# Performance work log

Measured on AMD Instinct MI355X. Metric: run time of the kernel, lower is better.

Reference implementation:

```python
import jax, jax.numpy as jnp
import numpy as np

U_DIM = 2048
V_DIM = 2048
LATENT = 2048
BATCH = 8192
SLOPE = 0.001  # LeakyReLU negative slope
EPS = 1e-5     # torch LayerNorm default eps


def layer_norm(x, gamma, beta):
    mu = jnp.mean(x, axis=-1, keepdims=True)
    var = jnp.var(x, axis=-1, keepdims=True)
    return (x - mu) * jax.lax.rsqrt(var + EPS) * gamma + beta


def leaky_relu(x):
    return jnp.where(x >= 0, x, SLOPE * x)


def setup_inputs() -> dict:
    key = jax.random.key(0)
    ks = jax.random.split(key, 6)
    u = jax.random.normal(ks[0], (BATCH, V_DIM), dtype=jnp.float32)
    v = jax.random.normal(ks[1], (BATCH, U_DIM), dtype=jnp.float32)
    # LayerNorm affine params (torch default: weight=1, bias=0 at init; randomize slightly)
    ln_u_w = jnp.ones((V_DIM,), jnp.float32)
    ln_u_b = jnp.zeros((V_DIM,), jnp.float32)
    ln_v_w = jnp.ones((U_DIM,), jnp.float32)
    ln_v_b = jnp.zeros((U_DIM,), jnp.float32)
    # Linear params (Kaiming-uniform-like scale)
    su = 1.0 / np.sqrt(V_DIM)
    sv = 1.0 / np.sqrt(U_DIM)
    W_u = jax.random.uniform(ks[2], (V_DIM, LATENT), jnp.float32, -su, su)
    b_u = jax.random.uniform(ks[3], (LATENT,), jnp.float32, -su, su)
    W_v = jax.random.uniform(ks[4], (U_DIM, LATENT), jnp.float32, -sv, sv)
    b_v = jax.random.uniform(ks[5], (LATENT,), jnp.float32, -sv, sv)
    return {"u": u, "v": v, "ln_u_w": ln_u_w, "ln_u_b": ln_u_b,
            "ln_v_w": ln_v_w, "ln_v_b": ln_v_b,
            "W_u": W_u, "b_u": b_u, "W_v": W_v, "b_v": b_v}


def reference(u, v, ln_u_w, ln_u_b, ln_v_w, ln_v_b, W_u, b_u, W_v, b_v):
    # u tower: LayerNorm -> Linear -> LeakyReLU
    hu = leaky_relu(layer_norm(u, ln_u_w, ln_u_b) @ W_u + b_u)   # [B, latent]
    # v tower: LayerNorm -> Linear -> LeakyReLU
    hv = leaky_relu(layer_norm(v, ln_v_w, ln_v_b) @ W_v + b_v)   # [B, latent]
    # dot-product reduction per row
    return jnp.sum(hu * hv, axis=-1)                              # [B]
```

## Files before the change

### kernel.cpp

```cpp
#include <hip/hip_runtime.h>

typedef unsigned short u16;
typedef __attribute__((ext_vector_type(8))) short short8;
typedef __attribute__((ext_vector_type(16))) float f32x16;

#define DIM 2048
#define NROWS 8192
#define SLOPE 0.001f
#define LN_EPS 1e-5f

#define LN_BLOCKS 4096
#define WT_BLOCKS 2048

#define BM 128
#define BN 256
#define BK 64
#define NT (DIM / BK)
#define TAUMAX (2 * NT)

__device__ __forceinline__ u16 f2bf(float f) {
    unsigned int u = __float_as_uint(f);
    u += 0x7FFFu + ((u >> 16) & 1u);
    return (u16)(u >> 16);
}

__device__ __forceinline__ void gload_lds16(const void* g, void* l) {
    __builtin_amdgcn_global_load_lds(
        (const __attribute__((address_space(1))) void*)g,
        (__attribute__((address_space(3))) void*)l, 16, 0, 0);
}

__global__ __launch_bounds__(256) void prep_kernel(
    const float* __restrict__ u, const float* __restrict__ v,
    const float* __restrict__ lnu_w, const float* __restrict__ lnu_b,
    const float* __restrict__ lnv_w, const float* __restrict__ lnv_b,
    const float* __restrict__ Wu, const float* __restrict__ Wv,
    u16* __restrict__ Au, u16* __restrict__ Av,
    u16* __restrict__ WtU, u16* __restrict__ WtV,
    float* __restrict__ out)
{
    __shared__ u16 tile[64][66];

    if (blockIdx.x < NROWS / 256)
        out[(blockIdx.x << 8) | threadIdx.x] = 0.f;

    if (blockIdx.x < LN_BLOCKS) {
        const int wave = threadIdx.x >> 6;
        const int lane = threadIdx.x & 63;
        const int r = blockIdx.x * 4 + wave;
        const bool isv = r >= NROWS;
        const int row = isv ? (r - NROWS) : r;
        const float* __restrict__ src = (isv ? v : u) + (size_t)row * DIM;
        const float* __restrict__ gw = isv ? lnv_w : lnu_w;
        const float* __restrict__ gb = isv ? lnv_b : lnu_b;
        u16* __restrict__ dst = (isv ? Av : Au) + (size_t)row * DIM;

        float4 x[8];
        #pragma unroll
        for (int i = 0; i < 8; ++i)
            x[i] = *(const float4*)(src + i * 256 + lane * 4);

        float s = 0.f, s2 = 0.f;
        #pragma unroll
        for (int i = 0; i < 8; ++i) {
            s  += (x[i].x + x[i].y) + (x[i].z + x[i].w);
            s2 += x[i].x*x[i].x + x[i].y*x[i].y + x[i].z*x[i].z + x[i].w*x[i].w;
        }
        #pragma unroll
        for (int m = 1; m < 64; m <<= 1) {
            s  += __shfl_xor(s, m);
            s2 += __shfl_xor(s2, m);
        }
        const float mu = s * (1.0f / DIM);
        const float rstd = rsqrtf(s2 * (1.0f / DIM) - mu * mu + LN_EPS);

        #pragma unroll
        for (int i = 0; i < 8; ++i) {
            const float4 w4 = *(const float4*)(gw + i * 256 + lane * 4);
            const float4 b4 = *(const float4*)(gb + i * 256 + lane * 4);
            union { u16 us[4]; uint2 v2; } pk;
            pk.us[0] = f2bf((x[i].x - mu) * rstd * w4.x + b4.x);
            pk.us[1] = f2bf((x[i].y - mu) * rstd * w4.y + b4.y);
            pk.us[2] = f2bf((x[i].z - mu) * rstd * w4.z + b4.z);
            pk.us[3] = f2bf((x[i].w - mu) * rstd * w4.w + b4.w);
            *(uint2*)(dst + i * 256 + lane * 4) = pk.v2;
        }
    } else {
        const int b = blockIdx.x - LN_BLOCKS;
        const int tower = b >> 10;
        const int t6 = b & 1023;
        const int n0 = (t6 & 31) * 64;
        const int k0 = (t6 >> 5) * 64;
        const float* __restrict__ src = tower ? Wv : Wu;
        u16* __restrict__ dst = tower ? WtV : WtU;
        const int c  = threadIdx.x & 15;
        const int rq = threadIdx.x >> 4;

        #pragma unroll
        for (int i = 0; i < 4; ++i) {
            const int k = rq + 16 * i;
            const float4 w = *(const float4*)(src + (size_t)(k0 + k) * DIM + n0 + c * 4);
            union { u16 us[4]; uint2 v2; } pk;
            pk.us[0] = f2bf(w.x); pk.us[1] = f2bf(w.y);
            pk.us[2] = f2bf(w.z); pk.us[3] = f2bf(w.w);
            *(uint2*)&tile[k][c * 4] = pk.v2;
        }
        __syncthreads();
        #pragma unroll
        for (int i = 0; i < 4; ++i) {
            const int n = rq + 16 * i;
            union { u16 us[4]; uint2 v2; } pk;
            #pragma unroll
            for (int j = 0; j < 4; ++j) pk.us[j] = tile[c * 4 + j][n];
            *(uint2*)(dst + (size_t)(n0 + n) * DIM + k0 + c * 4) = pk.v2;
        }
    }
}

__global__ __launch_bounds__(512) void fused_gemm_dot(
    const u16* __restrict__ Au, const u16* __restrict__ Av,
    const u16* __restrict__ WtU, const u16* __restrict__ WtV,
    const float* __restrict__ b_u, const float* __restrict__ b_v,
    float* __restrict__ out)
{
    __shared__ __align__(16) u16 smA[3][BM * BK];
    __shared__ __align__(16) u16 smB[3][BN * BK];

    const int tid   = threadIdx.x;
    const int wave  = tid >> 6;
    const int lane  = tid & 63;
    const int l31   = lane & 31;
    const int khalf = lane >> 5;
    const int wr    = wave >> 2;
    const int wc    = wave & 3;
    const int srow  = lane >> 3;
    const int gsw   = ((lane & 7) ^ srow ^ wave) * 8;

    const size_t arow0 = (size_t)blockIdx.x * BM;
    const size_t ncol0 = (size_t)blockIdx.y * BN;

#define STAGE_A(bi, tau) do {                                                      \
        const u16* As_ = (((tau) >> 5) ? Av : Au) + arow0 * DIM + ((tau)&31)*BK;   \
        _Pragma("unroll")                                                          \
        for (int i_ = 0; i_ < 2; ++i_) {                                           \
            const int rg_ = i_ * 64 + wave * 8;                                    \
            gload_lds16(As_ + (size_t)(rg_ + srow) * DIM + gsw,                    \
                        &smA[bi][rg_ * BK]);                                       \
        }                                                                          \
    } while (0)

#define STAGE_B(bi, tau, I0, I1) do {                                              \
        const u16* Bs_ = (((tau) >> 5) ? WtV : WtU) + ncol0 * DIM + ((tau)&31)*BK; \
        _Pragma("unroll")                                                          \
        for (int i_ = (I0); i_ < (I1); ++i_) {                                     \
            const int rg_ = i_ * 64 + wave * 8;                                    \
            gload_lds16(Bs_ + (size_t)(rg_ + srow) * DIM + gsw,                    \
                        &smB[bi][rg_ * BK]);                                       \
        }                                                                          \
    } while (0)

#define LDFRAGS(sa_, sb_, KK, X) do {                                              \
        const int cb_ = (KK) * 2 + khalf;                                          \
        _Pragma("unroll")                                                          \
        for (int mi_ = 0; mi_ < 2; ++mi_) {                                        \
            const int row_ = wr * 64 + mi_ * 32 + l31;                             \
            const int sl_ = cb_ ^ (row_ & 7) ^ ((row_ >> 3) & 7);                  \
            af[mi_][X] = *(const short8*)((sa_) + row_ * BK + sl_ * 8);            \
        }                                                                          \
        _Pragma("unroll")                                                          \
        for (int ni_ = 0; ni_ < 2; ++ni_) {                                        \
            const int row_ = wc * 64 + ni_ * 32 + l31;                             \
            const int sl_ = cb_ ^ (row_ & 7) ^ ((row_ >> 3) & 7);                  \
            bf[ni_][X] = *(const short8*)((sb_) + row_ * BK + sl_ * 8);            \
        }                                                                          \
    } while (0)

#define MFMA8() do {                                                               \
        __builtin_amdgcn_s_setprio(1);                                             \
        _Pragma("unroll")                                                          \
        for (int x_ = 0; x_ < 2; ++x_)                                             \
            _Pragma("unroll")                                                      \
            for (int mi_ = 0; mi_ < 2; ++mi_)                                      \
                _Pragma("unroll")                                                  \
                for (int ni_ = 0; ni_ < 2; ++ni_)                                  \
                    acc[mi_][ni_] = __builtin_amdgcn_mfma_f32_32x32x16_bf16(       \
                        af[mi_][x_], bf[ni_][x_], acc[mi_][ni_], 0, 0, 0);         \
        __builtin_amdgcn_s_setprio(0);                                             \
    } while (0)

    f32x16 acc[2][2];
    unsigned int hu_pk[2][2][8];

    STAGE_A(0, 0); STAGE_B(0, 0, 0, 4);
    STAGE_A(1, 1); STAGE_B(1, 1, 0, 4);

    int cur = 0;
    #pragma unroll
    for (int tower = 0; tower < 2; ++tower) {
        #pragma unroll
        for (int mi = 0; mi < 2; ++mi)
            #pragma unroll
            for (int ni = 0; ni < 2; ++ni)
                #pragma unroll
                for (int r = 0; r < 16; ++r)
                    acc[mi][ni][r] = 0.f;

        #pragma unroll 1
        for (int t = 0; t < NT; ++t) {
            const int tau = tower * NT + t;
            if (tau == TAUMAX - 1) asm volatile("s_waitcnt vmcnt(0)" ::: "memory");
            else                   asm volatile("s_waitcnt vmcnt(6)" ::: "memory");
            __builtin_amdgcn_s_barrier();
            asm volatile("" ::: "memory");

            const u16* sa = &smA[cur][0];
            const u16* sb = &smB[cur][0];
            int nb = cur + 2; if (nb >= 3) nb -= 3;
            short8 af[2][2], bf[2][2];

            LDFRAGS(sa, sb, 0, 0);
            LDFRAGS(sa, sb, 1, 1);
            if (tau + 2 < TAUMAX) { STAGE_A(nb, tau + 2); STAGE_B(nb, tau + 2, 0, 2); }
            __builtin_amdgcn_s_barrier();
            MFMA8();
            __builtin_amdgcn_s_barrier();
            LDFRAGS(sa, sb, 2, 0);
            LDFRAGS(sa, sb, 3, 1);
            if (tau + 2 < TAUMAX) STAGE_B(nb, tau + 2, 2, 4);
            __builtin_amdgcn_s_barrier();
            MFMA8();

            cur = (cur == 2) ? 0 : cur + 1;
        }

        if (tower == 0) {
            #pragma unroll
            for (int ni = 0; ni < 2; ++ni) {
                const float bias = b_u[ncol0 + wc * 64 + ni * 32 + l31];
                #pragma unroll
                for (int mi = 0; mi < 2; ++mi) {
                    #pragma unroll
                    for (int p = 0; p < 8; ++p) {
                        float h0 = acc[mi][ni][p * 2] + bias;
                        float h1 = acc[mi][ni][p * 2 + 1] + bias;
                        h0 = h0 >= 0.f ? h0 : SLOPE * h0;
                        h1 = h1 >= 0.f ? h1 : SLOPE * h1;
                        hu_pk[mi][ni][p] = (unsigned)f2bf(h0) | ((unsigned)f2bf(h1) << 16);
                    }
                }
            }
        }
    }

    #pragma unroll
    for (int mi = 0; mi < 2; ++mi) {
        #pragma unroll
        for (int rg = 0; rg < 4; ++rg) {
            float rsum[4] = {0.f, 0.f, 0.f, 0.f};
            #pragma unroll
            for (int ni = 0; ni < 2; ++ni) {
                const float bias = b_v[ncol0 + wc * 64 + ni * 32 + l31];
                #pragma unroll
                for (int r = 0; r < 4; ++r) {
                    const int reg = rg * 4 + r;
                    float hv = acc[mi][ni][reg] + bias;
                    hv = hv >= 0.f ? hv : SLOPE * hv;
                    const unsigned pk = hu_pk[mi][ni][reg >> 1];
                    const unsigned bits = (reg & 1) ? (pk & 0xFFFF0000u) : (pk << 16);
                    rsum[r] += __uint_as_float(bits) * hv;
                }
            }
            #pragma unroll
            for (int r = 0; r < 4; ++r) {
                const int reg = rg * 4 + r;
                float vsum = rsum[r];
                vsum += __shfl_xor(vsum, 1);
                vsum += __shfl_xor(vsum, 2);
                vsum += __shfl_xor(vsum, 4);
                vsum += __shfl_xor(vsum, 8);
                vsum += __shfl_xor(vsum, 16);
                if (l31 == 0) {
                    const int row = (int)arow0 + wr * 64 + mi * 32
                                  + (reg & 3) + 8 * (reg >> 2) + 4 * khalf;
                    atomicAdd(out + row, vsum);
                }
            }
        }
    }
#undef STAGE_A
#undef STAGE_B
#undef LDFRAGS
#undef MFMA8
}

extern "C" void kernel_launch(void* const* d_in, const int* in_sizes, int n_in,
                              void* d_out, int out_size, void* d_ws, size_t ws_size,
                              hipStream_t stream)
{
    const float* u     = (const float*)d_in[0];
    const float* v     = (const float*)d_in[1];
    const float* lnu_w = (const float*)d_in[2];
    const float* lnu_b = (const float*)d_in[3];
    const float* lnv_w = (const float*)d_in[4];
    const float* lnv_b = (const float*)d_in[5];
    const float* W_u   = (const float*)d_in[6];
    const float* b_u   = (const float*)d_in[7];
    const float* W_v   = (const float*)d_in[8];
    const float* b_v   = (const float*)d_in[9];
    float* out = (float*)d_out;

    char* ws = (char*)d_ws;
    u16* Au  = (u16*)(ws);
    u16* Av  = (u16*)(ws + (size_t)NROWS * DIM * 2);
    u16* WtU = (u16*)(ws + (size_t)NROWS * DIM * 4);
    u16* WtV = (u16*)(ws + (size_t)NROWS * DIM * 4 + (size_t)DIM * DIM * 2);

    prep_kernel<<<LN_BLOCKS + WT_BLOCKS, 256, 0, stream>>>(
        u, v, lnu_w, lnu_b, lnv_w, lnv_b, W_u, W_v, Au, Av, WtU, WtV, out);
    fused_gemm_dot<<<dim3(NROWS / BM, DIM / BN), 512, 0, stream>>>(
        Au, Av, WtU, WtV, b_u, b_v, out);
}
```

Baseline: 339.1 us.

## Enlarge GEMM tile to 256x256 with finer-grained phased staging pipeline

```diff
diff --git a/kernel.cpp b/kernel.cpp
--- a/kernel.cpp
+++ b/kernel.cpp
@@ -12,7 +12,7 @@
 #define LN_BLOCKS 4096
 #define WT_BLOCKS 2048
 
-#define BM 128
+#define BM 256
 #define BN 256
 #define BK 64
 #define NT (DIM / BK)
@@ -117,14 +117,14 @@
     }
 }
 
-__global__ __launch_bounds__(512) void fused_gemm_dot(
+__global__ __launch_bounds__(512, 2) void fused_gemm_dot(
     const u16* __restrict__ Au, const u16* __restrict__ Av,
     const u16* __restrict__ WtU, const u16* __restrict__ WtV,
     const float* __restrict__ b_u, const float* __restrict__ b_v,
     float* __restrict__ out)
 {
     __shared__ __align__(16) u16 smA[3][BM * BK];
-    __shared__ __align__(16) u16 smB[3][BN * BK];
+    __shared__ __align__(16) u16 smB[2][BN * BK];
 
     const int tid   = threadIdx.x;
     const int wave  = tid >> 6;
@@ -136,109 +136,120 @@
     const int srow  = lane >> 3;
     const int gsw   = ((lane & 7) ^ srow ^ wave) * 8;
 
-    const size_t arow0 = (size_t)blockIdx.x * BM;
-    const size_t ncol0 = (size_t)blockIdx.y * BN;
-
-#define STAGE_A(bi, tau) do {                                                      \
-        const u16* As_ = (((tau) >> 5) ? Av : Au) + arow0 * DIM + ((tau)&31)*BK;   \
-        _Pragma("unroll")                                                          \
-        for (int i_ = 0; i_ < 2; ++i_) {                                           \
-            const int rg_ = i_ * 64 + wave * 8;                                    \
-            gload_lds16(As_ + (size_t)(rg_ + srow) * DIM + gsw,                    \
-                        &smA[bi][rg_ * BK]);                                       \
+    const int bid = blockIdx.x;
+    const int bn  = bid & 7;
+    const int bm  = bid >> 3;
+    const size_t arow0 = (size_t)bm * BM;
+    const size_t ncol0 = (size_t)bn * BN;
+
+#define STAGE_A(T, buf, h) do {                                                    \
+        const u16* as_ = (((T) >= NT) ? Av : Au) + arow0 * DIM                     \
+                         + (size_t)((T) & (NT - 1)) * BK;                          \
+        _Pragma("unroll")                                                          \
+        for (int i2_ = 0; i2_ < 2; ++i2_) {                                        \
+            const int rg_ = (h) * 128 + i2_ * 64 + wave * 8;                       \
+            gload_lds16(as_ + (size_t)(rg_ + srow) * DIM + gsw,                    \
+                        &smA[buf][rg_ * BK]);                                      \
         }                                                                          \
     } while (0)
 
-#define STAGE_B(bi, tau, I0, I1) do {                                              \
-        const u16* Bs_ = (((tau) >> 5) ? WtV : WtU) + ncol0 * DIM + ((tau)&31)*BK; \
-        _Pragma("unroll")                                                          \
-        for (int i_ = (I0); i_ < (I1); ++i_) {                                     \
-            const int rg_ = i_ * 64 + wave * 8;                                    \
-            gload_lds16(Bs_ + (size_t)(rg_ + srow) * DIM + gsw,                    \
-                        &smB[bi][rg_ * BK]);                                       \
+#define STAGE_B(T, h) do {                                                         \
+        const u16* bs_ = (((T) >= NT) ? WtV : WtU) + ncol0 * DIM                   \
+                         + (size_t)((T) & (NT - 1)) * BK;                          \
+        _Pragma("unroll")                                                          \
+        for (int i2_ = 0; i2_ < 2; ++i2_) {                                        \
+            const int rg_ = (h) * 128 + i2_ * 64 + wave * 8;                       \
+            gload_lds16(bs_ + (size_t)(rg_ + srow) * DIM + gsw,                    \
+                        &smB[(T) & 1][rg_ * BK]);                                  \
         }                                                                          \
     } while (0)
 
-#define LDFRAGS(sa_, sb_, KK, X) do {                                              \
-        const int cb_ = (KK) * 2 + khalf;                                          \
-        _Pragma("unroll")                                                          \
-        for (int mi_ = 0; mi_ < 2; ++mi_) {                                        \
-            const int row_ = wr * 64 + mi_ * 32 + l31;                             \
+#define PHASE(AB, BB, KS, STAGE_STMT) do {                                         \
+        const u16* sa_ = &smA[AB][0];                                              \
+        const u16* sb_ = &smB[BB][0];                                              \
+        const int cb_ = (KS) * 2 + khalf;                                          \
+        short8 af_[4], bf_[2];                                                     \
+        _Pragma("unroll")                                                          \
+        for (int mi_ = 0; mi_ < 4; ++mi_) {                                        \
+            const int row_ = wr * 128 + mi_ * 32 + l31;                            \
             const int sl_ = cb_ ^ (row_ & 7) ^ ((row_ >> 3) & 7);                  \
-            af[mi_][X] = *(const short8*)((sa_) + row_ * BK + sl_ * 8);            \
+            af_[mi_] = *(const short8*)(sa_ + row_ * BK + sl_ * 8);                \
         }                                                                          \
         _Pragma("unroll")                                                          \
         for (int ni_ = 0; ni_ < 2; ++ni_) {                                        \
             const int row_ = wc * 64 + ni_ * 32 + l31;                             \
             const int sl_ = cb_ ^ (row_ & 7) ^ ((row_ >> 3) & 7);                  \
-            bf[ni_][X] = *(const short8*)((sb_) + row_ * BK + sl_ * 8);            \
+            bf_[ni_] = *(const short8*)(sb_ + row_ * BK + sl_ * 8);                \
         }                                                                          \
-    } while (0)
-
-#define MFMA8() do {                                                               \
+        STAGE_STMT;                                                                \
+        __builtin_amdgcn_s_barrier();                                              \
+        asm volatile("s_waitcnt lgkmcnt(0)" ::: "memory");                         \
         __builtin_amdgcn_s_setprio(1);                                             \
         _Pragma("unroll")                                                          \
-        for (int x_ = 0; x_ < 2; ++x_)                                             \
+        for (int mi_ = 0; mi_ < 4; ++mi_)                                          \
             _Pragma("unroll")                                                      \
-            for (int mi_ = 0; mi_ < 2; ++mi_)                                      \
-                _Pragma("unroll")                                                  \
-                for (int ni_ = 0; ni_ < 2; ++ni_)                                  \
-                    acc[mi_][ni_] = __builtin_amdgcn_mfma_f32_32x32x16_bf16(       \
-                        af[mi_][x_], bf[ni_][x_], acc[mi_][ni_], 0, 0, 0);         \
+            for (int ni_ = 0; ni_ < 2; ++ni_)                                      \
+                acc[mi_][ni_] = __builtin_amdgcn_mfma_f32_32x32x16_bf16(           \
+                    af_[mi_], bf_[ni_], acc[mi_][ni_], 0, 0, 0);                   \
         __builtin_amdgcn_s_setprio(0);                                             \
     } while (0)
 
-    f32x16 acc[2][2];
-    unsigned int hu_pk[2][2][8];
-
-    STAGE_A(0, 0); STAGE_B(0, 0, 0, 4);
-    STAGE_A(1, 1); STAGE_B(1, 1, 0, 4);
-
-    int cur = 0;
+    f32x16 acc[4][2];
+    unsigned int hu_pk[4][2][8];
+
     #pragma unroll
-    for (int tower = 0; tower < 2; ++tower) {
-        #pragma unroll
-        for (int mi = 0; mi < 2; ++mi)
-            #pragma unroll
-            for (int ni = 0; ni < 2; ++ni)
-                #pragma unroll
-                for (int r = 0; r < 16; ++r)
-                    acc[mi][ni][r] = 0.f;
-
-        #pragma unroll 1
-        for (int t = 0; t < NT; ++t) {
-            const int tau = tower * NT + t;
-            if (tau == TAUMAX - 1) asm volatile("s_waitcnt vmcnt(0)" ::: "memory");
-            else                   asm volatile("s_waitcnt vmcnt(6)" ::: "memory");
-            __builtin_amdgcn_s_barrier();
-            asm volatile("" ::: "memory");
-
-            const u16* sa = &smA[cur][0];
-            const u16* sb = &smB[cur][0];
-            int nb = cur + 2; if (nb >= 3) nb -= 3;
-            short8 af[2][2], bf[2][2];
-
-            LDFRAGS(sa, sb, 0, 0);
-            LDFRAGS(sa, sb, 1, 1);
-            if (tau + 2 < TAUMAX) { STAGE_A(nb, tau + 2); STAGE_B(nb, tau + 2, 0, 2); }
-            __builtin_amdgcn_s_barrier();
-            MFMA8();
-            __builtin_amdgcn_s_barrier();
-            LDFRAGS(sa, sb, 2, 0);
-            LDFRAGS(sa, sb, 3, 1);
-            if (tau + 2 < TAUMAX) STAGE_B(nb, tau + 2, 2, 4);
-            __builtin_amdgcn_s_barrier();
-            MFMA8();
-
-            cur = (cur == 2) ? 0 : cur + 1;
-        }
-
-        if (tower == 0) {
+    for (int mi = 0; mi < 4; ++mi)
+        #pragma unroll
+        for (int ni = 0; ni < 2; ++ni)
+            #pragma unroll
+            for (int r = 0; r < 16; ++r)
+                acc[mi][ni][r] = 0.f;
+
+    STAGE_A(0, 0, 0); STAGE_A(0, 0, 1);
+    STAGE_B(0, 0);    STAGE_B(0, 1);
+    STAGE_A(1, 1, 0); STAGE_A(1, 1, 1);
+    asm volatile("s_waitcnt vmcnt(4)" ::: "memory");
+    __builtin_amdgcn_s_barrier();
+    asm volatile("" ::: "memory");
+
+    int a0 = 0;
+    #pragma unroll 1
+    for (int i = 0; i < NT; ++i) {
+        const int tau = 2 * i;
+        const int a1 = (a0 + 1 < 3) ? a0 + 1 : a0 - 2;
+        const int a2 = (a0 + 2 < 3) ? a0 + 2 : a0 - 1;
+
+        PHASE(a0, 0, 0, { STAGE_B(tau + 1, 0); });
+        __builtin_amdgcn_s_barrier();
+        PHASE(a0, 0, 1, { STAGE_B(tau + 1, 1); });
+        __builtin_amdgcn_s_barrier();
+        PHASE(a0, 0, 2, { if (i < NT - 1) STAGE_A(tau + 2, a2, 0); });
+        __builtin_amdgcn_s_barrier();
+        PHASE(a0, 0, 3, { if (i < NT - 1) STAGE_A(tau + 2, a2, 1); });
+        if (i < NT - 1) asm volatile("s_waitcnt vmcnt(4)" ::: "memory");
+        else            asm volatile("s_waitcnt vmcnt(0)" ::: "memory");
+        __builtin_amdgcn_s_barrier();
+        asm volatile("" ::: "memory");
+
+        PHASE(a1, 1, 0, { if (i < NT - 1) STAGE_B(tau + 2, 0); });
+        __builtin_amdgcn_s_barrier();
+        PHASE(a1, 1, 1, { if (i < NT - 1) STAGE_B(tau + 2, 1); });
+        __builtin_amdgcn_s_barrier();
+        PHASE(a1, 1, 2, { if (i < NT - 1) STAGE_A(tau + 3, a0, 0); });
+        __builtin_amdgcn_s_barrier();
+        PHASE(a1, 1, 3, { if (i < NT - 1) STAGE_A(tau + 3, a0, 1); });
+        if (i < NT - 1) asm volatile("s_waitcnt vmcnt(4)" ::: "memory");
+        __builtin_amdgcn_s_barrier();
+        asm volatile("" ::: "memory");
+
+        a0 = a2;
+
+        if (i == 15) {
             #pragma unroll
             for (int ni = 0; ni < 2; ++ni) {
                 const float bias = b_u[ncol0 + wc * 64 + ni * 32 + l31];
                 #pragma unroll
-                for (int mi = 0; mi < 2; ++mi) {
+                for (int mi = 0; mi < 4; ++mi) {
                     #pragma unroll
                     for (int p = 0; p < 8; ++p) {
                         float h0 = acc[mi][ni][p * 2] + bias;
@@ -247,13 +258,15 @@
                         h1 = h1 >= 0.f ? h1 : SLOPE * h1;
                         hu_pk[mi][ni][p] = (unsigned)f2bf(h0) | ((unsigned)f2bf(h1) << 16);
                     }
+                    #pragma unroll
+                    for (int r = 0; r < 16; ++r) acc[mi][ni][r] = 0.f;
                 }
             }
         }
     }
 
     #pragma unroll
-    for (int mi = 0; mi < 2; ++mi) {
+    for (int mi = 0; mi < 4; ++mi) {
         #pragma unroll
         for (int rg = 0; rg < 4; ++rg) {
             float rsum[4] = {0.f, 0.f, 0.f, 0.f};
@@ -280,7 +293,7 @@
                 vsum += __shfl_xor(vsum, 8);
                 vsum += __shfl_xor(vsum, 16);
                 if (l31 == 0) {
-                    const int row = (int)arow0 + wr * 64 + mi * 32
+                    const int row = (int)arow0 + wr * 128 + mi * 32
                                   + (reg & 3) + 8 * (reg >> 2) + 4 * khalf;
                     atomicAdd(out + row, vsum);
                 }
@@ -289,8 +302,7 @@
     }
 #undef STAGE_A
 #undef STAGE_B
-#undef LDFRAGS
-#undef MFMA8
+#undef PHASE
 }
 
 extern "C" void kernel_launch(void* const* d_in, const int* in_sizes, int n_in,
@@ -317,6 +329,6 @@
 
     prep_kernel<<<LN_BLOCKS + WT_BLOCKS, 256, 0, stream>>>(
         u, v, lnu_w, lnu_b, lnv_w, lnv_b, W_u, W_v, Au, Av, WtU, WtV, out);
-    fused_gemm_dot<<<dim3(NROWS / BM, DIM / BN), 512, 0, stream>>>(
+    fused_gemm_dot<<<dim3((NROWS / BM) * (DIM / BN)), 512, 0, stream>>>(
         Au, Av, WtU, WtV, b_u, b_v, out);
 }
```

Result: slower. 371.6 us (+9.6%).
